# Optimization experiments

Measured on AMD Instinct MI355X. Metric: run time of the kernel, lower is better.

Reference implementation:

```python
import jax, jax.numpy as jnp
import numpy as np
import math

NUM_HEADS = 12
EMBED_DIM = 768

def setup_inputs() -> dict:
    key = jax.random.key(0)
    ks = jax.random.split(key, 9)
    B, T, D = 2, 2048, EMBED_DIM
    s = 1.0 / math.sqrt(D)
    inp = {
        "x": jax.random.normal(ks[0], (B, T, D), dtype=jnp.float32),
        "Wq": jax.random.normal(ks[1], (D, D), dtype=jnp.float32) * s,
        "bq": jnp.zeros((D,), dtype=jnp.float32),
        "Wk": jax.random.normal(ks[2], (D, D), dtype=jnp.float32) * s,
        "bk": jnp.zeros((D,), dtype=jnp.float32),
        "Wv": jax.random.normal(ks[3], (D, D), dtype=jnp.float32) * s,
        "bv": jnp.zeros((D,), dtype=jnp.float32),
        "Wo": jax.random.normal(ks[4], (D, D), dtype=jnp.float32) * s,
        "bo": jnp.zeros((D,), dtype=jnp.float32),
    }
    return inp

def reference(x, Wq, bq, Wk, bk, Wv, bv, Wo, bo):
    B, T, D = x.shape
    H = NUM_HEADS
    Dh = D // H
    # QKV projections, split heads: [B, H, T, Dh]
    def proj(W, b):
        y = x @ W.T + b
        return y.reshape(B, T, H, Dh).transpose(0, 2, 1, 3)
    q = proj(Wq, bq)
    k = proj(Wk, bk)
    v = proj(Wv, bv)
    scores = jnp.einsum('bhtd,bhsd->bhts', q, k) / math.sqrt(Dh)  # [B,H,T,T]
    attn = jax.nn.softmax(scores, axis=-1)
    ctx = jnp.einsum('bhts,bhsd->bhtd', attn, v)  # [B,H,T,Dh]
    ctx = ctx.transpose(0, 2, 1, 3).reshape(B, T, D)
    out = ctx @ Wo.T + bo
    return out
```

## Files before the change

kernel.cpp:

```cpp
#include <hip/hip_runtime.h>
#include <math.h>

using f32x4  = __attribute__((ext_vector_type(4))) float;
using bf16x8 = __attribute__((ext_vector_type(8))) short;

constexpr int Bb = 2;
constexpr int T  = 2048;
constexpr int D  = 768;
constexpr int H  = 12;
constexpr int Dh = 64;
constexpr int M  = Bb * T;
constexpr int NQKV = 3 * D;
#define SCALE_Q 0.18033688011112042f

__device__ __forceinline__ unsigned short f2bf(float f) {
    unsigned u = __float_as_uint(f);
    u += 0x7fffu + ((u >> 16) & 1u);
    return (unsigned short)(u >> 16);
}

__device__ __forceinline__ ushort4 f2bf4(float4 f) {
    return make_ushort4(f2bf(f.x), f2bf(f.y), f2bf(f.z), f2bf(f.w));
}

__device__ __forceinline__ void async_copy16(const void* g, void* lds_base) {
    __builtin_amdgcn_global_load_lds(
        (const __attribute__((address_space(1))) unsigned int*)g,
        (__attribute__((address_space(3))) unsigned int*)lds_base, 16, 0, 0);
}

__global__ __launch_bounds__(256) void prep_kernel(
    const float4* __restrict__ x,
    const float4* __restrict__ Wq, const float4* __restrict__ Wk,
    const float4* __restrict__ Wv, const float4* __restrict__ Wo,
    const float* __restrict__ bq, const float* __restrict__ bk, const float* __restrict__ bv,
    ushort4* __restrict__ Xb, ushort4* __restrict__ Wqkvb, ushort4* __restrict__ Wob,
    float* __restrict__ biasS)
{
    const int stride = gridDim.x * 256;
    const int i0 = blockIdx.x * 256 + threadIdx.x;
    const int NX = M * D / 4;
    const int NW = D * D / 4;
    for (int i = i0; i < NX; i += stride) Xb[i] = f2bf4(x[i]);
    for (int i = i0; i < NW; i += stride) {
        Wqkvb[i]          = f2bf4(Wq[i]);
        Wqkvb[NW + i]     = f2bf4(Wk[i]);
        Wqkvb[2 * NW + i] = f2bf4(Wv[i]);
        Wob[i]            = f2bf4(Wo[i]);
    }
    for (int i = i0; i < D; i += stride) {
        biasS[i]         = bq[i];
        biasS[D + i]     = bk[i];
        biasS[2 * D + i] = bv[i];
    }
}

template <int MODE>
__global__ __launch_bounds__(256) void gemm_bt_kernel(
    const unsigned short* __restrict__ A, const unsigned short* __restrict__ Bm,
    const float* __restrict__ bias, const int Kdim, const int Ndim,
    float* __restrict__ Cout,
    unsigned short* __restrict__ Qo, unsigned short* __restrict__ Ko,
    unsigned short* __restrict__ Vo)
{
    __shared__ unsigned short As[128 * 32];
    __shared__ unsigned short Bs[128 * 32];
    const int tid  = threadIdx.x;
    const int lane = tid & 63, wv = tid >> 6;
    const int l15  = lane & 15, l4 = lane >> 4;
    const int wr   = wv >> 1,  wc = wv & 1;
    const int row0 = blockIdx.y * 128, col0 = blockIdx.x * 128;

    f32x4 acc[4][4];
    #pragma unroll
    for (int i = 0; i < 4; ++i)
        #pragma unroll
        for (int j = 0; j < 4; ++j)
            acc[i][j] = (f32x4){0.f, 0.f, 0.f, 0.f};

    for (int k0 = 0; k0 < Kdim; k0 += 32) {
        __syncthreads();
        #pragma unroll
        for (int i = 0; i < 2; ++i) {
            const int offb = wv * 2048 + i * 1024;
            const int off  = offb + lane * 16;
            const int r = off >> 6, cb = off & 63;
            async_copy16(A  + (size_t)(row0 + r) * Kdim + k0 + (cb >> 1), (char*)As + offb);
            async_copy16(Bm + (size_t)(col0 + r) * Kdim + k0 + (cb >> 1), (char*)Bs + offb);
        }
        __syncthreads();

        bf16x8 af[4], bfr[4];
        #pragma unroll
        for (int i = 0; i < 4; ++i)
            af[i] = *(const bf16x8*)((const char*)As + (wr * 64 + i * 16 + l15) * 64 + l4 * 16);
        #pragma unroll
        for (int j = 0; j < 4; ++j)
            bfr[j] = *(const bf16x8*)((const char*)Bs + (wc * 64 + j * 16 + l15) * 64 + l4 * 16);
        #pragma unroll
        for (int i = 0; i < 4; ++i)
            #pragma unroll
            for (int j = 0; j < 4; ++j)
                acc[i][j] = __builtin_amdgcn_mfma_f32_16x16x32_bf16(af[i], bfr[j], acc[i][j], 0, 0, 0);
    }

    if (MODE == 0) {
        #pragma unroll
        for (int j = 0; j < 4; ++j) {
            const int n = col0 + wc * 64 + j * 16 + l15;
            const float bv_ = bias[n];
            #pragma unroll
            for (int i = 0; i < 4; ++i) {
                #pragma unroll
                for (int r = 0; r < 4; ++r) {
                    const int m = row0 + wr * 64 + i * 16 + l4 * 4 + r;
                    Cout[(size_t)m * Ndim + n] = acc[i][j][r] + bv_;
                }
            }
        }
    } else {
        #pragma unroll
        for (int j = 0; j < 4; ++j) {
            const int n = col0 + wc * 64 + j * 16 + l15;
            const int which = n / D;
            const int hd = n % D;
            const int h = hd >> 6, d = hd & 63;
            const float bv_ = bias[n];
            if (which == 2) {
                #pragma unroll
                for (int i = 0; i < 4; ++i) {
                    const int m0 = row0 + wr * 64 + i * 16 + l4 * 4;
                    const int b = m0 >> 11, t = m0 & (T - 1);
                    float4 v4;
                    v4.x = acc[i][j][0] + bv_; v4.y = acc[i][j][1] + bv_;
                    v4.z = acc[i][j][2] + bv_; v4.w = acc[i][j][3] + bv_;
                    *(ushort4*)&Vo[((size_t)(b * H + h) * Dh + d) * T + t] = f2bf4(v4);
                }
            } else {
                const float scale = (which == 0) ? SCALE_Q : 1.0f;
                unsigned short* dst = (which == 0) ? Qo : Ko;
                #pragma unroll
                for (int i = 0; i < 4; ++i) {
                    #pragma unroll
                    for (int r = 0; r < 4; ++r) {
                        const int m = row0 + wr * 64 + i * 16 + l4 * 4 + r;
                        const int b = m >> 11, t = m & (T - 1);
                        dst[((size_t)(b * H + h) * T + t) * Dh + d] =
                            f2bf((acc[i][j][r] + bv_) * scale);
                    }
                }
            }
        }
    }
}

__global__ __launch_bounds__(256) void attn_kernel(
    const unsigned short* __restrict__ Q, const unsigned short* __restrict__ Kg,
    const unsigned short* __restrict__ Vt, unsigned short* __restrict__ Ctx)
{
    __shared__ unsigned short Ks[2][64 * 64];
    __shared__ unsigned short Vs[2][64 * 64];
    __shared__ unsigned short Ps[64 * 64];
    const int bh = blockIdx.y;
    const int q0 = blockIdx.x * 64;
    const int tid = threadIdx.x, lane = tid & 63, wv = tid >> 6;
    const int l15 = lane & 15, l4 = lane >> 4;
    const unsigned short* Qp = Q  + (size_t)bh * T * Dh;
    const unsigned short* Kp = Kg + (size_t)bh * T * Dh;
    const unsigned short* Vp = Vt + (size_t)bh * Dh * T;

    bf16x8 qf[2];
    #pragma unroll
    for (int ks = 0; ks < 2; ++ks)
        qf[ks] = *(const bf16x8*)&Qp[(size_t)(q0 + wv * 16 + l15) * Dh + ks * 32 + l4 * 8];

    const short oneb = (short)0x3F80;
    const bf16x8 onesf = {oneb, oneb, oneb, oneb, oneb, oneb, oneb, oneb};

    auto load_tiles = [&](int kt, int buf) {
        #pragma unroll
        for (int i = 0; i < 2; ++i) {
            const int offb = wv * 2048 + i * 1024;
            const int off  = offb + lane * 16;
            const int r = off >> 7;
            const int blk = (off & 127) >> 4;
            const int gc = (blk ^ (r & 7)) << 3;
            async_copy16(Kp + (size_t)(kt + r) * Dh + gc, (char*)&Ks[buf][0] + offb);
            async_copy16(Vp + (size_t)r * T + kt + gc,    (char*)&Vs[buf][0] + offb);
        }
    };

    load_tiles(0, 0);
    f32x4 o[4], oL;
    #pragma unroll
    for (int nj = 0; nj < 4; ++nj) o[nj] = (f32x4){0.f, 0.f, 0.f, 0.f};
    oL = (f32x4){0.f, 0.f, 0.f, 0.f};

    for (int kt64 = 0; kt64 < T / 64; ++kt64) {
        const int cur = kt64 & 1;
        __syncthreads();
        if (kt64 + 1 < T / 64) load_tiles((kt64 + 1) * 64, cur ^ 1);

        f32x4 s[4];
        #pragma unroll
        for (int nj = 0; nj < 4; ++nj) s[nj] = (f32x4){0.f, 0.f, 0.f, 0.f};
        #pragma unroll
        for (int ks = 0; ks < 2; ++ks) {
            #pragma unroll
            for (int nj = 0; nj < 4; ++nj) {
                bf16x8 kb = *(const bf16x8*)((const char*)&Ks[cur][0] +
                        (nj * 16 + l15) * 128 + (((ks << 2) + l4) ^ (l15 & 7)) * 16);
                s[nj] = __builtin_amdgcn_mfma_f32_16x16x32_bf16(qf[ks], kb, s[nj], 0, 0, 0);
            }
        }

        #pragma unroll
        for (int nj = 0; nj < 4; ++nj) {
            #pragma unroll
            for (int r = 0; r < 4; ++r) {
                const float p = __builtin_amdgcn_exp2f(fminf(s[nj][r], 80.0f));
                const int row = wv * 16 + l4 * 4 + r;
                const int blk = (nj * 2 + (l15 >> 3)) ^ (row & 7);
                *(unsigned short*)((char*)Ps + row * 128 + blk * 16 + (l15 & 7) * 2) =
                    (unsigned short)(__float_as_uint(p) >> 16);
            }
        }

        #pragma unroll
        for (int ks = 0; ks < 2; ++ks) {
            bf16x8 pa = *(const bf16x8*)((const char*)Ps +
                    (wv * 16 + l15) * 128 + (((ks << 2) + l4) ^ (l15 & 7)) * 16);
            oL = __builtin_amdgcn_mfma_f32_16x16x32_bf16(pa, onesf, oL, 0, 0, 0);
            #pragma unroll
            for (int nj = 0; nj < 4; ++nj) {
                bf16x8 vb = *(const bf16x8*)((const char*)&Vs[cur][0] +
                        (nj * 16 + l15) * 128 + (((ks << 2) + l4) ^ (l15 & 7)) * 16);
                o[nj] = __builtin_amdgcn_mfma_f32_16x16x32_bf16(pa, vb, o[nj], 0, 0, 0);
            }
        }
    }

    const int b = bh / H, h = bh % H;
    #pragma unroll
    for (int r = 0; r < 4; ++r) {
        const float inv = 1.0f / oL[r];
        const int t = q0 + wv * 16 + l4 * 4 + r;
        #pragma unroll
        for (int nj = 0; nj < 4; ++nj) {
            const int col = h * 64 + nj * 16 + l15;
            Ctx[(size_t)(b * T + t) * D + col] = f2bf(o[nj][r] * inv);
        }
    }
}

extern "C" void kernel_launch(void* const* d_in, const int* in_sizes, int n_in,
                              void* d_out, int out_size, void* d_ws, size_t ws_size,
                              hipStream_t stream) {
    const float* x  = (const float*)d_in[0];
    const float* Wq = (const float*)d_in[1];
    const float* bq = (const float*)d_in[2];
    const float* Wk = (const float*)d_in[3];
    const float* bk = (const float*)d_in[4];
    const float* Wv = (const float*)d_in[5];
    const float* bv = (const float*)d_in[6];
    const float* Wo = (const float*)d_in[7];
    const float* bo = (const float*)d_in[8];
    float* out = (float*)d_out;

    char* w = (char*)d_ws;
    auto alloc = [&](size_t bytes) {
        char* p = w; w += (bytes + 255) & ~(size_t)255; return p;
    };
    unsigned short* Xb    = (unsigned short*)alloc((size_t)M * D * 2);
    unsigned short* Wqkvb = (unsigned short*)alloc((size_t)NQKV * D * 2);
    unsigned short* Wob   = (unsigned short*)alloc((size_t)D * D * 2);
    float*          biasS = (float*)alloc((size_t)NQKV * 4);
    unsigned short* Qb    = (unsigned short*)alloc((size_t)M * D * 2);
    unsigned short* Kb    = (unsigned short*)alloc((size_t)M * D * 2);
    unsigned short* Vtb   = (unsigned short*)alloc((size_t)M * D * 2);
    unsigned short* Ctxb  = (unsigned short*)alloc((size_t)M * D * 2);

    prep_kernel<<<1024, 256, 0, stream>>>(
        (const float4*)x, (const float4*)Wq, (const float4*)Wk, (const float4*)Wv,
        (const float4*)Wo, bq, bk, bv,
        (ushort4*)Xb, (ushort4*)Wqkvb, (ushort4*)Wob, biasS);

    gemm_bt_kernel<1><<<dim3(NQKV / 128, M / 128), 256, 0, stream>>>(
        Xb, Wqkvb, biasS, D, NQKV, nullptr, Qb, Kb, Vtb);

    attn_kernel<<<dim3(T / 64, Bb * H), 256, 0, stream>>>(Qb, Kb, Vtb, Ctxb);

    gemm_bt_kernel<0><<<dim3(D / 128, M / 128), 256, 0, stream>>>(
        Ctxb, Wob, bo, D, D, out, nullptr, nullptr, nullptr);
}
```

Before: 190.1 us.

## Rewrite attention with 32x32 MFMA, register-resident P and permuted V layout

The attention kernel switches from 16x16x32 to 32x32x16 MFMA with 2 waves of 32 query rows each, computing S^T so the exp'd probabilities stay in registers and are packed directly as the A operand for the PV product. V is written by the QKV GEMM with a permuted t index so those register fragments line up with V's K dimension. This removes the LDS round trip for P and the ones-vector MFMA for row sums, which are now accumulated in scalar adds and shuffles. Halving the block size lowers per-block parallelism and drops the exp clamp, which could overflow for large scores.

```diff
diff --git a/kernel.cpp b/kernel.cpp
--- a/kernel.cpp
+++ b/kernel.cpp
@@ -1,8 +1,9 @@
 #include <hip/hip_runtime.h>
 #include <math.h>
 
-using f32x4  = __attribute__((ext_vector_type(4))) float;
-using bf16x8 = __attribute__((ext_vector_type(8))) short;
+using f32x4   = __attribute__((ext_vector_type(4))) float;
+using f32x16  = __attribute__((ext_vector_type(16))) float;
+using bf16x8  = __attribute__((ext_vector_type(8))) short;
 
 constexpr int Bb = 2;
 constexpr int T  = 2048;
@@ -21,6 +22,13 @@
 
 __device__ __forceinline__ ushort4 f2bf4(float4 f) {
     return make_ushort4(f2bf(f.x), f2bf(f.y), f2bf(f.z), f2bf(f.w));
+}
+
+__device__ __forceinline__ unsigned rnepk(float a, float b) {
+    unsigned ua = __float_as_uint(a), ub = __float_as_uint(b);
+    ua += 0x7fffu + ((ua >> 16) & 1u);
+    ub += 0x7fffu + ((ub >> 16) & 1u);
+    return (ub & 0xffff0000u) | (ua >> 16);
 }
 
 __device__ __forceinline__ void async_copy16(const void* g, void* lds_base) {
@@ -131,10 +139,12 @@
                 for (int i = 0; i < 4; ++i) {
                     const int m0 = row0 + wr * 64 + i * 16 + l4 * 4;
                     const int b = m0 >> 11, t = m0 & (T - 1);
+                    int w = t & 12; w = ((w << 1) | (w >> 1)) & 12;
+                    const int tp = (t & ~12) | w;
                     float4 v4;
                     v4.x = acc[i][j][0] + bv_; v4.y = acc[i][j][1] + bv_;
                     v4.z = acc[i][j][2] + bv_; v4.w = acc[i][j][3] + bv_;
-                    *(ushort4*)&Vo[((size_t)(b * H + h) * Dh + d) * T + t] = f2bf4(v4);
+                    *(ushort4*)&Vo[((size_t)(b * H + h) * Dh + d) * T + tp] = f2bf4(v4);
                 }
             } else {
                 const float scale = (which == 0) ? SCALE_Q : 1.0f;
@@ -154,102 +164,108 @@
     }
 }
 
-__global__ __launch_bounds__(256) void attn_kernel(
+__global__ __launch_bounds__(128) void attn_kernel(
     const unsigned short* __restrict__ Q, const unsigned short* __restrict__ Kg,
     const unsigned short* __restrict__ Vt, unsigned short* __restrict__ Ctx)
 {
     __shared__ unsigned short Ks[2][64 * 64];
     __shared__ unsigned short Vs[2][64 * 64];
-    __shared__ unsigned short Ps[64 * 64];
+    __shared__ float linv[64];
     const int bh = blockIdx.y;
     const int q0 = blockIdx.x * 64;
     const int tid = threadIdx.x, lane = tid & 63, wv = tid >> 6;
-    const int l15 = lane & 15, l4 = lane >> 4;
+    const int l31 = lane & 31, l5 = lane >> 5;
     const unsigned short* Qp = Q  + (size_t)bh * T * Dh;
     const unsigned short* Kp = Kg + (size_t)bh * T * Dh;
     const unsigned short* Vp = Vt + (size_t)bh * Dh * T;
 
-    bf16x8 qf[2];
+    bf16x8 qf[4];
     #pragma unroll
-    for (int ks = 0; ks < 2; ++ks)
-        qf[ks] = *(const bf16x8*)&Qp[(size_t)(q0 + wv * 16 + l15) * Dh + ks * 32 + l4 * 8];
-
-    const short oneb = (short)0x3F80;
-    const bf16x8 onesf = {oneb, oneb, oneb, oneb, oneb, oneb, oneb, oneb};
+    for (int c = 0; c < 4; ++c)
+        qf[c] = *(const bf16x8*)&Qp[(size_t)(q0 + wv * 32 + l31) * Dh + c * 16 + l5 * 8];
 
     auto load_tiles = [&](int kt, int buf) {
         #pragma unroll
-        for (int i = 0; i < 2; ++i) {
-            const int offb = wv * 2048 + i * 1024;
+        for (int i = 0; i < 4; ++i) {
+            const int offb = wv * 4096 + i * 1024;
             const int off  = offb + lane * 16;
-            const int r = off >> 7;
-            const int blk = (off & 127) >> 4;
-            const int gc = (blk ^ (r & 7)) << 3;
+            const int r  = off >> 7;
+            const int bl = (off & 127) >> 4;
+            const int gc = (bl ^ (r & 7)) << 3;
             async_copy16(Kp + (size_t)(kt + r) * Dh + gc, (char*)&Ks[buf][0] + offb);
             async_copy16(Vp + (size_t)r * T + kt + gc,    (char*)&Vs[buf][0] + offb);
         }
     };
 
     load_tiles(0, 0);
-    f32x4 o[4], oL;
-    #pragma unroll
-    for (int nj = 0; nj < 4; ++nj) o[nj] = (f32x4){0.f, 0.f, 0.f, 0.f};
-    oL = (f32x4){0.f, 0.f, 0.f, 0.f};
+    f32x16 o0 = {}, o1 = {};
+    float lpart = 0.f;
 
     for (int kt64 = 0; kt64 < T / 64; ++kt64) {
         const int cur = kt64 & 1;
         __syncthreads();
         if (kt64 + 1 < T / 64) load_tiles((kt64 + 1) * 64, cur ^ 1);
 
-        f32x4 s[4];
-        #pragma unroll
-        for (int nj = 0; nj < 4; ++nj) s[nj] = (f32x4){0.f, 0.f, 0.f, 0.f};
-        #pragma unroll
-        for (int ks = 0; ks < 2; ++ks) {
-            #pragma unroll
-            for (int nj = 0; nj < 4; ++nj) {
-                bf16x8 kb = *(const bf16x8*)((const char*)&Ks[cur][0] +
-                        (nj * 16 + l15) * 128 + (((ks << 2) + l4) ^ (l15 & 7)) * 16);
-                s[nj] = __builtin_amdgcn_mfma_f32_16x16x32_bf16(qf[ks], kb, s[nj], 0, 0, 0);
+        const char* Kb = (const char*)&Ks[cur][0];
+        const char* Vb = (const char*)&Vs[cur][0];
+        const int swz = ((l5) ^ (l31 & 7));
+
+        f32x16 s0 = {}, s1 = {};
+        #pragma unroll
+        for (int c = 0; c < 4; ++c) {
+            const int blk = ((2 * c + l5) ^ (l31 & 7)) << 4;
+            bf16x8 kb0 = *(const bf16x8*)(Kb + l31 * 128 + blk);
+            bf16x8 kb1 = *(const bf16x8*)(Kb + (32 + l31) * 128 + blk);
+            s0 = __builtin_amdgcn_mfma_f32_32x32x16_bf16(kb0, qf[c], s0, 0, 0, 0);
+            s1 = __builtin_amdgcn_mfma_f32_32x32x16_bf16(kb1, qf[c], s1, 0, 0, 0);
+        }
+
+        float ls = 0.f;
+        #pragma unroll
+        for (int r = 0; r < 16; ++r) {
+            s0[r] = __builtin_amdgcn_exp2f(s0[r]);
+            s1[r] = __builtin_amdgcn_exp2f(s1[r]);
+            ls += s0[r] + s1[r];
+        }
+        lpart += ls;
+
+        #pragma unroll
+        for (int c = 0; c < 4; ++c) {
+            union { unsigned u[4]; bf16x8 v; } pu;
+            if (c < 2) {
+                const int b0 = (c & 1) * 8;
+                pu.u[0] = rnepk(s0[b0 + 0], s0[b0 + 1]);
+                pu.u[1] = rnepk(s0[b0 + 2], s0[b0 + 3]);
+                pu.u[2] = rnepk(s0[b0 + 4], s0[b0 + 5]);
+                pu.u[3] = rnepk(s0[b0 + 6], s0[b0 + 7]);
+            } else {
+                const int b0 = (c & 1) * 8;
+                pu.u[0] = rnepk(s1[b0 + 0], s1[b0 + 1]);
+                pu.u[1] = rnepk(s1[b0 + 2], s1[b0 + 3]);
+                pu.u[2] = rnepk(s1[b0 + 4], s1[b0 + 5]);
+                pu.u[3] = rnepk(s1[b0 + 6], s1[b0 + 7]);
             }
-        }
-
-        #pragma unroll
-        for (int nj = 0; nj < 4; ++nj) {
-            #pragma unroll
-            for (int r = 0; r < 4; ++r) {
-                const float p = __builtin_amdgcn_exp2f(fminf(s[nj][r], 80.0f));
-                const int row = wv * 16 + l4 * 4 + r;
-                const int blk = (nj * 2 + (l15 >> 3)) ^ (row & 7);
-                *(unsigned short*)((char*)Ps + row * 128 + blk * 16 + (l15 & 7) * 2) =
-                    (unsigned short)(__float_as_uint(p) >> 16);
-            }
-        }
-
-        #pragma unroll
-        for (int ks = 0; ks < 2; ++ks) {
-            bf16x8 pa = *(const bf16x8*)((const char*)Ps +
-                    (wv * 16 + l15) * 128 + (((ks << 2) + l4) ^ (l15 & 7)) * 16);
-            oL = __builtin_amdgcn_mfma_f32_16x16x32_bf16(pa, onesf, oL, 0, 0, 0);
-            #pragma unroll
-            for (int nj = 0; nj < 4; ++nj) {
-                bf16x8 vb = *(const bf16x8*)((const char*)&Vs[cur][0] +
-                        (nj * 16 + l15) * 128 + (((ks << 2) + l4) ^ (l15 & 7)) * 16);
-                o[nj] = __builtin_amdgcn_mfma_f32_16x16x32_bf16(pa, vb, o[nj], 0, 0, 0);
-            }
-        }
-    }
+            const int blk = ((2 * c + l5) ^ (l31 & 7)) << 4;
+            bf16x8 vb0 = *(const bf16x8*)(Vb + l31 * 128 + blk);
+            bf16x8 vb1 = *(const bf16x8*)(Vb + (32 + l31) * 128 + blk);
+            o0 = __builtin_amdgcn_mfma_f32_32x32x16_bf16(pu.v, vb0, o0, 0, 0, 0);
+            o1 = __builtin_amdgcn_mfma_f32_32x32x16_bf16(pu.v, vb1, o1, 0, 0, 0);
+        }
+        (void)swz;
+    }
+
+    const float lfull = lpart + __shfl_xor(lpart, 32);
+    if (l5 == 0) linv[wv * 32 + l31] = 1.0f / lfull;
 
     const int b = bh / H, h = bh % H;
     #pragma unroll
-    for (int r = 0; r < 4; ++r) {
-        const float inv = 1.0f / oL[r];
-        const int t = q0 + wv * 16 + l4 * 4 + r;
-        #pragma unroll
-        for (int nj = 0; nj < 4; ++nj) {
-            const int col = h * 64 + nj * 16 + l15;
-            Ctx[(size_t)(b * T + t) * D + col] = f2bf(o[nj][r] * inv);
-        }
+    for (int reg = 0; reg < 16; ++reg) {
+        const int qb = wv * 32 + (reg & 3) + 8 * (reg >> 2) + 4 * l5;
+        const float inv = linv[qb];
+        const int t = q0 + qb;
+        const size_t base = ((size_t)(b * T + t)) * D + h * 64 + l31;
+        Ctx[base]      = f2bf(o0[reg] * inv);
+        Ctx[base + 32] = f2bf(o1[reg] * inv);
     }
 }
 
@@ -288,7 +304,7 @@
     gemm_bt_kernel<1><<<dim3(NQKV / 128, M / 128), 256, 0, stream>>>(
         Xb, Wqkvb, biasS, D, NQKV, nullptr, Qb, Kb, Vtb);
 
-    attn_kernel<<<dim3(T / 64, Bb * H), 256, 0, stream>>>(Qb, Kb, Vtb, Ctxb);
+    attn_kernel<<<dim3(T / 64, Bb * H), 128, 0, stream>>>(Qb, Kb, Vtb, Ctxb);
 
     gemm_bt_kernel<0><<<dim3(D / 128, M / 128), 256, 0, stream>>>(
         Ctxb, Wob, bo, D, D, out, nullptr, nullptr, nullptr);
```

New measurement: 193.3 us. About the same (+1.7%).
